# Performance work log

Hardware: AMD Instinct MI355X
Metric: run time of the kernel (lower is better)

Reference implementation:

```python
import jax, jax.numpy as jnp
import numpy as np

MODEL_DIM = 1024
RANK = 128

def setup_inputs() -> dict:
    key = jax.random.key(0)
    k1, k2 = jax.random.split(key)
    batch = jax.random.normal(k1, (8, 512, MODEL_DIM), dtype=jnp.float32)
    # nn.init.uniform_(proj, -0.05, 0.05)
    proj = jax.random.uniform(k2, (MODEL_DIM, RANK), dtype=jnp.float32, minval=-0.05, maxval=0.05)
    return {"batch": batch, "proj": proj}

def reference(batch, proj):
    # project: (B, S, D) @ (D, R) -> (B, S, R)
    transformed = jnp.matmul(batch, proj)
    # all-pairs squared L2 distance via broadcast diff, matching the torch math
    # diffs: (B, S, S, R)
    diffs = transformed[:, :, None, :] - transformed[:, None, :, :]
    squared_distances = jnp.sum(diffs * diffs, axis=-1)  # (B, S, S)
    return squared_distances
```

## Files before the change

### kernel.cpp

```cpp
#include <hip/hip_runtime.h>

#define SEQ 512
#define MD  1024
#define RK  128

typedef __attribute__((ext_vector_type(8))) short  bf16x8;
typedef __attribute__((ext_vector_type(4))) float  floatx4;
typedef __attribute__((ext_vector_type(4))) unsigned int uint4v;
typedef __attribute__((ext_vector_type(4))) unsigned short ushortx4;

__device__ inline unsigned short f2bf(float f) {
    union { float f; unsigned u; } v; v.f = f;
    unsigned r = v.u + 0x7fffu + ((v.u >> 16) & 1u);
    return (unsigned short)(r >> 16);
}

__global__ __launch_bounds__(256) void proj_t(
    const float* __restrict__ proj, unsigned short* __restrict__ PT)
{
    const int tid = blockIdx.x * 256 + threadIdx.x;
    const int n   = tid & 127;
    const int kc  = (tid >> 7) * 8;
    unsigned short tmp[8];
    #pragma unroll
    for (int j = 0; j < 8; ++j)
        tmp[j] = f2bf(proj[(size_t)(kc + j) * RK + n]);
    *(bf16x8*)(PT + (size_t)n * MD + kc) = *(bf16x8*)tmp;
}

#define LDA 1032

__global__ __launch_bounds__(512, 2) void proj_rows(
    const float* __restrict__ batch, const unsigned short* __restrict__ PT,
    unsigned short* __restrict__ T, float* __restrict__ Nrm)
{
    __shared__ unsigned short As[16 * LDA];
    __shared__ float Np[8][16];

    const int t    = threadIdx.x;
    const int w    = t >> 6;
    const int l    = t & 63;
    const int lm   = l & 15;
    const int quad = l >> 4;
    const int r0   = blockIdx.x * 16;

    {
        const int row = t >> 5, kb = (t & 31) * 8;
        const float* src = batch + (size_t)(r0 + row) * MD + kb;
        unsigned short* dst = As + row * LDA + kb;
        #pragma unroll
        for (int c = 0; c < 4; ++c) {
            float4 f0 = *(const float4*)(src + c * 256);
            float4 f1 = *(const float4*)(src + c * 256 + 4);
            unsigned short tmp[8];
            tmp[0] = f2bf(f0.x); tmp[1] = f2bf(f0.y);
            tmp[2] = f2bf(f0.z); tmp[3] = f2bf(f0.w);
            tmp[4] = f2bf(f1.x); tmp[5] = f2bf(f1.y);
            tmp[6] = f2bf(f1.z); tmp[7] = f2bf(f1.w);
            *(bf16x8*)(dst + c * 256) = *(bf16x8*)tmp;
        }
    }
    __syncthreads();

    floatx4 acc = (floatx4){0.f, 0.f, 0.f, 0.f};
    const unsigned short* aptr = As + lm * LDA + quad * 8;
    const unsigned short* bptr = PT + (size_t)(w * 16 + lm) * MD + quad * 8;

    #pragma unroll
    for (int s = 0; s < 32; ++s) {
        bf16x8 av = *(const bf16x8*)(aptr + s * 32);
        bf16x8 bv = *(const bf16x8*)(bptr + s * 32);
        acc = __builtin_amdgcn_mfma_f32_16x16x32_bf16(av, bv, acc, 0, 0, 0);
    }

    #pragma unroll
    for (int r = 0; r < 4; ++r) {
        float v = acc[r];
        T[(size_t)(r0 + quad * 4 + r) * RK + w * 16 + lm] = f2bf(v);
        float p = v * v;
        p += __shfl_xor(p, 1, 64);
        p += __shfl_xor(p, 2, 64);
        p += __shfl_xor(p, 4, 64);
        p += __shfl_xor(p, 8, 64);
        if (lm == 0) Np[w][quad * 4 + r] = p;
    }
    __syncthreads();

    if (t < 16) {
        float s = 0.f;
        #pragma unroll
        for (int ww = 0; ww < 8; ++ww) s += Np[ww][t];
        Nrm[r0 + t] = s;
    }
}

#define LDB 136

__global__ __launch_bounds__(256) void dist_mfma(
    const unsigned short* __restrict__ T, const float* __restrict__ Nrm,
    float* __restrict__ out)
{
    __shared__ unsigned short Ti[64 * LDB];
    __shared__ unsigned short Tj[64 * LDB];
    __shared__ float nI[64], nJ[64];

    const int t    = threadIdx.x;
    const int w    = t >> 6;
    const int l    = t & 63;
    const int lm   = l & 15;
    const int quad = l >> 4;
    const int jt = blockIdx.x, it = blockIdx.y, b = blockIdx.z;
    const int i0 = it * 64, j0 = jt * 64;
    const unsigned short* Tb = T + (size_t)b * SEQ * RK;

    {
        int row = t >> 2, kq = (t & 3) * 32;
        const unsigned short* si = Tb + (size_t)(i0 + row) * RK + kq;
        const unsigned short* sj = Tb + (size_t)(j0 + row) * RK + kq;
        #pragma unroll
        for (int q = 0; q < 4; ++q) {
            *(uint4v*)(Ti + row * LDB + kq + q * 8) = *(const uint4v*)(si + q * 8);
            *(uint4v*)(Tj + row * LDB + kq + q * 8) = *(const uint4v*)(sj + q * 8);
        }
        if (t < 64)       nI[t]      = Nrm[(size_t)b * SEQ + i0 + t];
        else if (t < 128) nJ[t - 64] = Nrm[(size_t)b * SEQ + j0 + (t - 64)];
    }
    __syncthreads();

    floatx4 acc[4];
    #pragma unroll
    for (int i = 0; i < 4; ++i) acc[i] = (floatx4){0.f, 0.f, 0.f, 0.f};

    #pragma unroll
    for (int s = 0; s < 4; ++s) {
        bf16x8 av = *(const bf16x8*)(Ti + (w * 16 + lm) * LDB + s * 32 + quad * 8);
        #pragma unroll
        for (int nt = 0; nt < 4; ++nt) {
            bf16x8 bv = *(const bf16x8*)(Tj + (nt * 16 + lm) * LDB + s * 32 + quad * 8);
            acc[nt] = __builtin_amdgcn_mfma_f32_16x16x32_bf16(av, bv, acc[nt], 0, 0, 0);
        }
    }

    float niv[4];
    #pragma unroll
    for (int r = 0; r < 4; ++r) niv[r] = nI[w * 16 + quad * 4 + r];

    float* ob = out + ((size_t)b * SEQ + (i0 + w * 16)) * SEQ + j0;
    #pragma unroll
    for (int nt = 0; nt < 4; ++nt) {
        float njv = nJ[nt * 16 + lm];
        #pragma unroll
        for (int r = 0; r < 4; ++r) {
            ob[(size_t)(quad * 4 + r) * SEQ + nt * 16 + lm] =
                niv[r] + njv - 2.f * acc[nt][r];
        }
    }
}

extern "C" void kernel_launch(void* const* d_in, const int* in_sizes, int n_in,
                              void* d_out, int out_size, void* d_ws, size_t ws_size,
                              hipStream_t stream) {
    const float* batch = (const float*)d_in[0];
    const float* proj  = (const float*)d_in[1];
    float* out = (float*)d_out;

    unsigned short* T   = (unsigned short*)d_ws;
    float*          Nrm = (float*)((char*)d_ws + (1 << 20));
    unsigned short* PT  = (unsigned short*)((char*)d_ws + (1 << 20) + (1 << 16));

    proj_t   <<<64,  256, 0, stream>>>(proj, PT);
    proj_rows<<<256, 512, 0, stream>>>(batch, PT, T, Nrm);
    dist_mfma<<<dim3(8, 8, 8), 256, 0, stream>>>(T, Nrm, out);
}
```

Measured before the change: 78.71 us.

## Fuse three kernels into one cooperative persistent kernel with grid syncs

Merges the proj transpose, row projection and distance kernels into a single cooperative launch of 512 blocks, using grid-wide syncs between phases. The aim is to remove two kernel launch boundaries and their gaps. The projection phase now uses 256-thread blocks computing two MFMA tiles per wave, and the distance phase reads T and norms straight from global memory with no LDS staging. Grid syncs cost time of their own, and only 256 of the 512 blocks work in the projection phase. If the cooperative launch fails, the code falls back to three launches.

```diff
diff --git a/kernel.cpp b/kernel.cpp
--- a/kernel.cpp
+++ b/kernel.cpp
@@ -1,12 +1,15 @@
 #include <hip/hip_runtime.h>
+#include <hip/hip_cooperative_groups.h>
+
+namespace cg = cooperative_groups;
 
 #define SEQ 512
 #define MD  1024
 #define RK  128
+#define LDA 1032
 
 typedef __attribute__((ext_vector_type(8))) short  bf16x8;
 typedef __attribute__((ext_vector_type(4))) float  floatx4;
-typedef __attribute__((ext_vector_type(4))) unsigned int uint4v;
 typedef __attribute__((ext_vector_type(4))) unsigned short ushortx4;
 
 __device__ inline unsigned short f2bf(float f) {
@@ -15,144 +18,126 @@
     return (unsigned short)(r >> 16);
 }
 
-__global__ __launch_bounds__(256) void proj_t(
-    const float* __restrict__ proj, unsigned short* __restrict__ PT)
-{
-    const int tid = blockIdx.x * 256 + threadIdx.x;
-    const int n   = tid & 127;
-    const int kc  = (tid >> 7) * 8;
-    unsigned short tmp[8];
-    #pragma unroll
-    for (int j = 0; j < 8; ++j)
-        tmp[j] = f2bf(proj[(size_t)(kc + j) * RK + n]);
-    *(bf16x8*)(PT + (size_t)n * MD + kc) = *(bf16x8*)tmp;
-}
-
-#define LDA 1032
-
-__global__ __launch_bounds__(512, 2) void proj_rows(
-    const float* __restrict__ batch, const unsigned short* __restrict__ PT,
-    unsigned short* __restrict__ T, float* __restrict__ Nrm)
+__global__ __launch_bounds__(256, 2) void fused_all(
+    const float* __restrict__ batch, const float* __restrict__ proj,
+    float* __restrict__ out, unsigned short* __restrict__ T,
+    float* __restrict__ Nrm, unsigned short* __restrict__ PT, int mode)
 {
     __shared__ unsigned short As[16 * LDA];
-    __shared__ float Np[8][16];
+    __shared__ float Np[4][16];
 
     const int t    = threadIdx.x;
+    const int lb   = blockIdx.x;
     const int w    = t >> 6;
     const int l    = t & 63;
     const int lm   = l & 15;
     const int quad = l >> 4;
-    const int r0   = blockIdx.x * 16;
 
-    {
-        const int row = t >> 5, kb = (t & 31) * 8;
-        const float* src = batch + (size_t)(r0 + row) * MD + kb;
-        unsigned short* dst = As + row * LDA + kb;
-        #pragma unroll
-        for (int c = 0; c < 4; ++c) {
-            float4 f0 = *(const float4*)(src + c * 256);
-            float4 f1 = *(const float4*)(src + c * 256 + 4);
+    if (mode < 0 || mode == 0) {
+        const int gid = lb * 256 + t;
+        if (gid < 16384) {
+            const int n  = gid & 127;
+            const int kc = (gid >> 7) * 8;
             unsigned short tmp[8];
-            tmp[0] = f2bf(f0.x); tmp[1] = f2bf(f0.y);
-            tmp[2] = f2bf(f0.z); tmp[3] = f2bf(f0.w);
-            tmp[4] = f2bf(f1.x); tmp[5] = f2bf(f1.y);
-            tmp[6] = f2bf(f1.z); tmp[7] = f2bf(f1.w);
-            *(bf16x8*)(dst + c * 256) = *(bf16x8*)tmp;
+            #pragma unroll
+            for (int j = 0; j < 8; ++j)
+                tmp[j] = f2bf(proj[(size_t)(kc + j) * RK + n]);
+            *(bf16x8*)(PT + (size_t)n * MD + kc) = *(bf16x8*)tmp;
         }
     }
-    __syncthreads();
+    if (mode < 0) { __threadfence(); cg::this_grid().sync(); }
 
-    floatx4 acc = (floatx4){0.f, 0.f, 0.f, 0.f};
-    const unsigned short* aptr = As + lm * LDA + quad * 8;
-    const unsigned short* bptr = PT + (size_t)(w * 16 + lm) * MD + quad * 8;
+    if ((mode < 0 || mode == 1) && lb < 256) {
+        const int r0 = lb * 16;
 
-    #pragma unroll
-    for (int s = 0; s < 32; ++s) {
-        bf16x8 av = *(const bf16x8*)(aptr + s * 32);
-        bf16x8 bv = *(const bf16x8*)(bptr + s * 32);
-        acc = __builtin_amdgcn_mfma_f32_16x16x32_bf16(av, bv, acc, 0, 0, 0);
+        {
+            const int row = t >> 4, c0 = (t & 15) * 8;
+            const float* src = batch + (size_t)(r0 + row) * MD + c0;
+            unsigned short* dst = As + row * LDA + c0;
+            #pragma unroll
+            for (int c = 0; c < 8; ++c) {
+                float4 f0 = *(const float4*)(src + c * 128);
+                float4 f1 = *(const float4*)(src + c * 128 + 4);
+                unsigned short tmp[8];
+                tmp[0] = f2bf(f0.x); tmp[1] = f2bf(f0.y);
+                tmp[2] = f2bf(f0.z); tmp[3] = f2bf(f0.w);
+                tmp[4] = f2bf(f1.x); tmp[5] = f2bf(f1.y);
+                tmp[6] = f2bf(f1.z); tmp[7] = f2bf(f1.w);
+                *(bf16x8*)(dst + c * 128) = *(bf16x8*)tmp;
+            }
+        }
+        __syncthreads();
+
+        floatx4 acc0 = (floatx4){0.f, 0.f, 0.f, 0.f};
+        floatx4 acc1 = (floatx4){0.f, 0.f, 0.f, 0.f};
+        const unsigned short* aptr = As + lm * LDA + quad * 8;
+        const unsigned short* b0 = PT + (size_t)(w * 32 + lm) * MD + quad * 8;
+        const unsigned short* b1 = b0 + (size_t)16 * MD;
+
+        #pragma unroll
+        for (int s = 0; s < 32; ++s) {
+            bf16x8 av = *(const bf16x8*)(aptr + s * 32);
+            acc0 = __builtin_amdgcn_mfma_f32_16x16x32_bf16(
+                av, *(const bf16x8*)(b0 + s * 32), acc0, 0, 0, 0);
+            acc1 = __builtin_amdgcn_mfma_f32_16x16x32_bf16(
+                av, *(const bf16x8*)(b1 + s * 32), acc1, 0, 0, 0);
+        }
+
+        #pragma unroll
+        for (int r = 0; r < 4; ++r) {
+            const float v0 = acc0[r], v1 = acc1[r];
+            const int row = r0 + quad * 4 + r;
+            T[(size_t)row * RK + w * 32 + lm]      = f2bf(v0);
+            T[(size_t)row * RK + w * 32 + 16 + lm] = f2bf(v1);
+            float p = v0 * v0 + v1 * v1;
+            p += __shfl_xor(p, 1, 64);
+            p += __shfl_xor(p, 2, 64);
+            p += __shfl_xor(p, 4, 64);
+            p += __shfl_xor(p, 8, 64);
+            if (lm == 0) Np[w][quad * 4 + r] = p;
+        }
+        __syncthreads();
+        if (t < 16)
+            Nrm[r0 + t] = Np[0][t] + Np[1][t] + Np[2][t] + Np[3][t];
     }
+    if (mode < 0) { __threadfence(); cg::this_grid().sync(); }
 
-    #pragma unroll
-    for (int r = 0; r < 4; ++r) {
-        float v = acc[r];
-        T[(size_t)(r0 + quad * 4 + r) * RK + w * 16 + lm] = f2bf(v);
-        float p = v * v;
-        p += __shfl_xor(p, 1, 64);
-        p += __shfl_xor(p, 2, 64);
-        p += __shfl_xor(p, 4, 64);
-        p += __shfl_xor(p, 8, 64);
-        if (lm == 0) Np[w][quad * 4 + r] = p;
-    }
-    __syncthreads();
+    if (mode < 0 || mode == 2) {
+        const int jt = lb & 7, it = (lb >> 3) & 7, b = lb >> 6;
+        const int i0 = it * 64, j0 = jt * 64;
+        const unsigned short* Tb = T + (size_t)b * SEQ * RK;
 
-    if (t < 16) {
-        float s = 0.f;
+        floatx4 acc[4];
         #pragma unroll
-        for (int ww = 0; ww < 8; ++ww) s += Np[ww][t];
-        Nrm[r0 + t] = s;
-    }
-}
+        for (int i = 0; i < 4; ++i) acc[i] = (floatx4){0.f, 0.f, 0.f, 0.f};
 
-#define LDB 136
+        const unsigned short* ap = Tb + (size_t)(i0 + w * 16 + lm) * RK + quad * 8;
+        const unsigned short* bp = Tb + (size_t)(j0 + lm) * RK + quad * 8;
 
-__global__ __launch_bounds__(256) void dist_mfma(
-    const unsigned short* __restrict__ T, const float* __restrict__ Nrm,
-    float* __restrict__ out)
-{
-    __shared__ unsigned short Ti[64 * LDB];
-    __shared__ unsigned short Tj[64 * LDB];
-    __shared__ float nI[64], nJ[64];
+        #pragma unroll
+        for (int s = 0; s < 4; ++s) {
+            bf16x8 av = *(const bf16x8*)(ap + s * 32);
+            #pragma unroll
+            for (int nt = 0; nt < 4; ++nt) {
+                bf16x8 bv = *(const bf16x8*)(bp + (size_t)nt * 16 * RK + s * 32);
+                acc[nt] = __builtin_amdgcn_mfma_f32_16x16x32_bf16(av, bv, acc[nt], 0, 0, 0);
+            }
+        }
 
-    const int t    = threadIdx.x;
-    const int w    = t >> 6;
-    const int l    = t & 63;
-    const int lm   = l & 15;
-    const int quad = l >> 4;
-    const int jt = blockIdx.x, it = blockIdx.y, b = blockIdx.z;
-    const int i0 = it * 64, j0 = jt * 64;
-    const unsigned short* Tb = T + (size_t)b * SEQ * RK;
+        const float* NI = Nrm + (size_t)b * SEQ;
+        float niv[4];
+        #pragma unroll
+        for (int r = 0; r < 4; ++r) niv[r] = NI[i0 + w * 16 + quad * 4 + r];
 
-    {
-        int row = t >> 2, kq = (t & 3) * 32;
-        const unsigned short* si = Tb + (size_t)(i0 + row) * RK + kq;
-        const unsigned short* sj = Tb + (size_t)(j0 + row) * RK + kq;
-        #pragma unroll
-        for (int q = 0; q < 4; ++q) {
-            *(uint4v*)(Ti + row * LDB + kq + q * 8) = *(const uint4v*)(si + q * 8);
-            *(uint4v*)(Tj + row * LDB + kq + q * 8) = *(const uint4v*)(sj + q * 8);
-        }
-        if (t < 64)       nI[t]      = Nrm[(size_t)b * SEQ + i0 + t];
-        else if (t < 128) nJ[t - 64] = Nrm[(size_t)b * SEQ + j0 + (t - 64)];
-    }
-    __syncthreads();
-
-    floatx4 acc[4];
-    #pragma unroll
-    for (int i = 0; i < 4; ++i) acc[i] = (floatx4){0.f, 0.f, 0.f, 0.f};
-
-    #pragma unroll
-    for (int s = 0; s < 4; ++s) {
-        bf16x8 av = *(const bf16x8*)(Ti + (w * 16 + lm) * LDB + s * 32 + quad * 8);
+        float* ob = out + ((size_t)b * SEQ + (i0 + w * 16)) * SEQ + j0;
         #pragma unroll
         for (int nt = 0; nt < 4; ++nt) {
-            bf16x8 bv = *(const bf16x8*)(Tj + (nt * 16 + lm) * LDB + s * 32 + quad * 8);
-            acc[nt] = __builtin_amdgcn_mfma_f32_16x16x32_bf16(av, bv, acc[nt], 0, 0, 0);
-        }
-    }
-
-    float niv[4];
-    #pragma unroll
-    for (int r = 0; r < 4; ++r) niv[r] = nI[w * 16 + quad * 4 + r];
-
-    float* ob = out + ((size_t)b * SEQ + (i0 + w * 16)) * SEQ + j0;
-    #pragma unroll
-    for (int nt = 0; nt < 4; ++nt) {
-        float njv = nJ[nt * 16 + lm];
-        #pragma unroll
-        for (int r = 0; r < 4; ++r) {
-            ob[(size_t)(quad * 4 + r) * SEQ + nt * 16 + lm] =
-                niv[r] + njv - 2.f * acc[nt][r];
+            const float njv = NI[j0 + nt * 16 + lm];
+            #pragma unroll
+            for (int r = 0; r < 4; ++r) {
+                ob[(size_t)(quad * 4 + r) * SEQ + nt * 16 + lm] =
+                    niv[r] + njv - 2.f * acc[nt][r];
+            }
         }
     }
 }
@@ -168,7 +153,16 @@
     float*          Nrm = (float*)((char*)d_ws + (1 << 20));
     unsigned short* PT  = (unsigned short*)((char*)d_ws + (1 << 20) + (1 << 16));
 
-    proj_t   <<<64,  256, 0, stream>>>(proj, PT);
-    proj_rows<<<256, 512, 0, stream>>>(batch, PT, T, Nrm);
-    dist_mfma<<<dim3(8, 8, 8), 256, 0, stream>>>(T, Nrm, out);
+    int mode = -1;
+    void* args[] = { (void*)&batch, (void*)&proj, (void*)&out,
+                     (void*)&T, (void*)&Nrm, (void*)&PT, (void*)&mode };
+
+    hipError_t err = hipLaunchCooperativeKernel(
+        (void*)fused_all, dim3(512), dim3(256), args, 0, stream);
+
+    if (err != hipSuccess) {
+        fused_all<<<64,  256, 0, stream>>>(batch, proj, out, T, Nrm, PT, 0);
+        fused_all<<<256, 256, 0, stream>>>(batch, proj, out, T, Nrm, PT, 1);
+        fused_all<<<512, 256, 0, stream>>>(batch, proj, out, T, Nrm, PT, 2);
+    }
 }
```

Result: slower. 311.9 us (+296.2%).

## Drop proj transpose kernel and LDS staging in distance kernel

Applied to the files above, without the earlier changes.

Removes the separate proj transpose/convert kernel. proj_rows now reads fp32 proj directly with strided loads and converts each B fragment to bf16 inside the MFMA loop. The distance kernel no longer stages T tiles and norms in shared memory or synchronises; it loads MFMA fragments straight from global memory (relying on cache) and uses a flattened 1D grid. This saves one launch and LDS traffic, but each proj_rows block repeats the fp32 conversion and issues scalar strided global loads for B.

```diff
diff --git a/kernel.cpp b/kernel.cpp
--- a/kernel.cpp
+++ b/kernel.cpp
@@ -3,11 +3,10 @@
 #define SEQ 512
 #define MD  1024
 #define RK  128
+#define LDA 1032
 
 typedef __attribute__((ext_vector_type(8))) short  bf16x8;
 typedef __attribute__((ext_vector_type(4))) float  floatx4;
-typedef __attribute__((ext_vector_type(4))) unsigned int uint4v;
-typedef __attribute__((ext_vector_type(4))) unsigned short ushortx4;
 
 __device__ inline unsigned short f2bf(float f) {
     union { float f; unsigned u; } v; v.f = f;
@@ -15,23 +14,8 @@
     return (unsigned short)(r >> 16);
 }
 
-__global__ __launch_bounds__(256) void proj_t(
-    const float* __restrict__ proj, unsigned short* __restrict__ PT)
-{
-    const int tid = blockIdx.x * 256 + threadIdx.x;
-    const int n   = tid & 127;
-    const int kc  = (tid >> 7) * 8;
-    unsigned short tmp[8];
-    #pragma unroll
-    for (int j = 0; j < 8; ++j)
-        tmp[j] = f2bf(proj[(size_t)(kc + j) * RK + n]);
-    *(bf16x8*)(PT + (size_t)n * MD + kc) = *(bf16x8*)tmp;
-}
-
-#define LDA 1032
-
 __global__ __launch_bounds__(512, 2) void proj_rows(
-    const float* __restrict__ batch, const unsigned short* __restrict__ PT,
+    const float* __restrict__ batch, const float* __restrict__ proj,
     unsigned short* __restrict__ T, float* __restrict__ Nrm)
 {
     __shared__ unsigned short As[16 * LDA];
@@ -45,9 +29,9 @@
     const int r0   = blockIdx.x * 16;
 
     {
-        const int row = t >> 5, kb = (t & 31) * 8;
-        const float* src = batch + (size_t)(r0 + row) * MD + kb;
-        unsigned short* dst = As + row * LDA + kb;
+        const int row = t >> 5, c0 = (t & 31) * 8;
+        const float* src = batch + (size_t)(r0 + row) * MD + c0;
+        unsigned short* dst = As + row * LDA + c0;
         #pragma unroll
         for (int c = 0; c < 4; ++c) {
             float4 f0 = *(const float4*)(src + c * 256);
@@ -64,18 +48,22 @@
 
     floatx4 acc = (floatx4){0.f, 0.f, 0.f, 0.f};
     const unsigned short* aptr = As + lm * LDA + quad * 8;
-    const unsigned short* bptr = PT + (size_t)(w * 16 + lm) * MD + quad * 8;
+    const float* bbase = proj + (size_t)(quad * 8) * RK + w * 16 + lm;
 
     #pragma unroll
     for (int s = 0; s < 32; ++s) {
         bf16x8 av = *(const bf16x8*)(aptr + s * 32);
-        bf16x8 bv = *(const bf16x8*)(bptr + s * 32);
-        acc = __builtin_amdgcn_mfma_f32_16x16x32_bf16(av, bv, acc, 0, 0, 0);
+        const float* bp = bbase + (size_t)s * 32 * RK;
+        unsigned short btmp[8];
+        #pragma unroll
+        for (int j = 0; j < 8; ++j) btmp[j] = f2bf(bp[(size_t)j * RK]);
+        acc = __builtin_amdgcn_mfma_f32_16x16x32_bf16(
+            av, *(bf16x8*)btmp, acc, 0, 0, 0);
     }
 
     #pragma unroll
     for (int r = 0; r < 4; ++r) {
-        float v = acc[r];
+        const float v = acc[r];
         T[(size_t)(r0 + quad * 4 + r) * RK + w * 16 + lm] = f2bf(v);
         float p = v * v;
         p += __shfl_xor(p, 1, 64);
@@ -94,61 +82,46 @@
     }
 }
 
-#define LDB 136
-
 __global__ __launch_bounds__(256) void dist_mfma(
     const unsigned short* __restrict__ T, const float* __restrict__ Nrm,
     float* __restrict__ out)
 {
-    __shared__ unsigned short Ti[64 * LDB];
-    __shared__ unsigned short Tj[64 * LDB];
-    __shared__ float nI[64], nJ[64];
-
     const int t    = threadIdx.x;
     const int w    = t >> 6;
     const int l    = t & 63;
     const int lm   = l & 15;
     const int quad = l >> 4;
-    const int jt = blockIdx.x, it = blockIdx.y, b = blockIdx.z;
+    const int lb   = blockIdx.x;
+    const int jt = lb & 7, it = (lb >> 3) & 7, b = lb >> 6;
     const int i0 = it * 64, j0 = jt * 64;
     const unsigned short* Tb = T + (size_t)b * SEQ * RK;
-
-    {
-        int row = t >> 2, kq = (t & 3) * 32;
-        const unsigned short* si = Tb + (size_t)(i0 + row) * RK + kq;
-        const unsigned short* sj = Tb + (size_t)(j0 + row) * RK + kq;
-        #pragma unroll
-        for (int q = 0; q < 4; ++q) {
-            *(uint4v*)(Ti + row * LDB + kq + q * 8) = *(const uint4v*)(si + q * 8);
-            *(uint4v*)(Tj + row * LDB + kq + q * 8) = *(const uint4v*)(sj + q * 8);
-        }
-        if (t < 64)       nI[t]      = Nrm[(size_t)b * SEQ + i0 + t];
-        else if (t < 128) nJ[t - 64] = Nrm[(size_t)b * SEQ + j0 + (t - 64)];
-    }
-    __syncthreads();
 
     floatx4 acc[4];
     #pragma unroll
     for (int i = 0; i < 4; ++i) acc[i] = (floatx4){0.f, 0.f, 0.f, 0.f};
 
+    const unsigned short* ap = Tb + (size_t)(i0 + w * 16 + lm) * RK + quad * 8;
+    const unsigned short* bp = Tb + (size_t)(j0 + lm) * RK + quad * 8;
+
     #pragma unroll
     for (int s = 0; s < 4; ++s) {
-        bf16x8 av = *(const bf16x8*)(Ti + (w * 16 + lm) * LDB + s * 32 + quad * 8);
+        bf16x8 av = *(const bf16x8*)(ap + s * 32);
         #pragma unroll
         for (int nt = 0; nt < 4; ++nt) {
-            bf16x8 bv = *(const bf16x8*)(Tj + (nt * 16 + lm) * LDB + s * 32 + quad * 8);
+            bf16x8 bv = *(const bf16x8*)(bp + (size_t)nt * 16 * RK + s * 32);
             acc[nt] = __builtin_amdgcn_mfma_f32_16x16x32_bf16(av, bv, acc[nt], 0, 0, 0);
         }
     }
 
+    const float* NI = Nrm + (size_t)b * SEQ;
     float niv[4];
     #pragma unroll
-    for (int r = 0; r < 4; ++r) niv[r] = nI[w * 16 + quad * 4 + r];
+    for (int r = 0; r < 4; ++r) niv[r] = NI[i0 + w * 16 + quad * 4 + r];
 
     float* ob = out + ((size_t)b * SEQ + (i0 + w * 16)) * SEQ + j0;
     #pragma unroll
     for (int nt = 0; nt < 4; ++nt) {
-        float njv = nJ[nt * 16 + lm];
+        const float njv = NI[j0 + nt * 16 + lm];
         #pragma unroll
         for (int r = 0; r < 4; ++r) {
             ob[(size_t)(quad * 4 + r) * SEQ + nt * 16 + lm] =
@@ -166,9 +139,7 @@
 
     unsigned short* T   = (unsigned short*)d_ws;
     float*          Nrm = (float*)((char*)d_ws + (1 << 20));
-    unsigned short* PT  = (unsigned short*)((char*)d_ws + (1 << 20) + (1 << 16));
 
-    proj_t   <<<64,  256, 0, stream>>>(proj, PT);
-    proj_rows<<<256, 512, 0, stream>>>(batch, PT, T, Nrm);
-    dist_mfma<<<dim3(8, 8, 8), 256, 0, stream>>>(T, Nrm, out);
+    proj_rows<<<256, 512, 0, stream>>>(batch, proj, T, Nrm);
+    dist_mfma<<<512, 256, 0, stream>>>(T, Nrm, out);
 }
```

Result: slower. 80.31 us (+2.0%).
